# Kernel optimization log

Hardware: AMD Instinct MI355X
Metric: run time of the kernel (lower is better)

## Reference

```python
import jax, jax.numpy as jnp
import numpy as np
from jax.ops import segment_sum

N_NODES = 200000
N_EDGES = 3200000
N_GRAPHS = 400
IN_FEATS = 32
DIMS = [(32, 128), (128, 48), (48, 28), (28, 5)]  # (in, out) per SAGEConv layer


def setup_inputs() -> dict:
    key = jax.random.key(0)
    ks = jax.random.split(key, 4 + 3 * len(DIMS))
    inp = {
        'feat': jax.random.normal(ks[0], (N_NODES, IN_FEATS), dtype=jnp.float32),
        'src': jax.random.randint(ks[1], (N_EDGES,), 0, N_NODES),
        'dst': jax.random.randint(ks[2], (N_EDGES,), 0, N_NODES),
        'graph_ids': jnp.sort(jax.random.randint(ks[3], (N_NODES,), 0, N_GRAPHS)),
    }
    for i, (d_in, d_out) in enumerate(DIMS):
        s = 1.0 / np.sqrt(d_in)
        inp[f'W_self{i}'] = jax.random.uniform(ks[4 + 3 * i], (d_in, d_out), jnp.float32, -s, s)
        inp[f'W_neigh{i}'] = jax.random.uniform(ks[5 + 3 * i], (d_in, d_out), jnp.float32, -s, s)
        inp[f'b{i}'] = jax.random.uniform(ks[6 + 3 * i], (d_out,), jnp.float32, -s, s)
    return inp


def _sage_mean(h, src, dst, W_neigh, W_self, b):
    # mean-aggregate in-neighbor features, then project: fc_self(h) + fc_neigh(mean_u->v h_u) + b
    deg = segment_sum(jnp.ones((src.shape[0],), h.dtype), dst, num_segments=N_NODES)
    agg = segment_sum(h[src], dst, num_segments=N_NODES)  # [N, d_in] irregular gather+scatter
    agg = agg / jnp.maximum(deg, 1.0)[:, None]            # zero for isolated nodes (DGL semantics)
    return h @ W_self + agg @ W_neigh + b


def reference(feat, src, dst, graph_ids,
              W_self0, W_neigh0, b0, W_self1, W_neigh1, b1,
              W_self2, W_neigh2, b2, W_self3, W_neigh3, b3):
    h = jax.nn.relu(_sage_mean(feat, src, dst, W_neigh0, W_self0, b0))
    h = jax.nn.relu(_sage_mean(h, src, dst, W_neigh1, W_self1, b1))
    h = jax.nn.relu(_sage_mean(h, src, dst, W_neigh2, W_self2, b2))
    h = _sage_mean(h, src, dst, W_neigh3, W_self3, b3)
    # dgl.mean_nodes: per-graph mean readout
    cnt = segment_sum(jnp.ones((N_NODES,), h.dtype), graph_ids, num_segments=N_GRAPHS)
    tot = segment_sum(h, graph_ids, num_segments=N_GRAPHS)
    return tot / jnp.maximum(cnt, 1.0)[:, None]
```

## Files before the change

### kernel.cpp

```cpp
#include <hip/hip_runtime.h>

#define NN 200000
#define NE 3200000
#define NG 400
#define NB 196
#define BSHIFT 8
#define NBKT 782
#define EPB 12500
#define SRCMASK 0x3FFFF

__global__ void hist_bkt(const int* __restrict__ dst, int* __restrict__ bcnt) {
    __shared__ int h[NBKT];
    for (int i = threadIdx.x; i < NBKT; i += 256) h[i] = 0;
    __syncthreads();
    int stride = gridDim.x * blockDim.x;
    for (int e = blockIdx.x * blockDim.x + threadIdx.x; e < NE; e += stride)
        atomicAdd(&h[dst[e] >> BSHIFT], 1);
    __syncthreads();
    for (int i = threadIdx.x; i < NBKT; i += 256)
        if (h[i]) atomicAdd(&bcnt[i], h[i]);
}

__global__ void scan_bkt(const int* __restrict__ bcnt, int* __restrict__ bbase,
                         int* __restrict__ bcur) {
    __shared__ int sh[256];
    int t = threadIdx.x;
    int v[4]; int own = 0;
    #pragma unroll
    for (int i = 0; i < 4; ++i) {
        int idx = t * 4 + i;
        v[i] = (idx < NBKT) ? bcnt[idx] : 0;
        own += v[i];
    }
    sh[t] = own; __syncthreads();
    for (int off = 1; off < 256; off <<= 1) {
        int x = (t >= off) ? sh[t - off] : 0;
        __syncthreads();
        sh[t] += x;
        __syncthreads();
    }
    int excl = sh[t] - own;
    #pragma unroll
    for (int i = 0; i < 4; ++i) {
        int idx = t * 4 + i;
        if (idx < NBKT) { bbase[idx] = excl; bcur[idx] = excl; excl += v[i]; }
    }
}

__global__ void partition_pairs(const int* __restrict__ src, const int* __restrict__ dst,
                                int* __restrict__ bcur, unsigned int* __restrict__ pairs) {
    __shared__ int h[NBKT];
    __shared__ int base[NBKT];
    int e0 = blockIdx.x * EPB;
    int e1 = min(e0 + EPB, NE);
    for (int i = threadIdx.x; i < NBKT; i += 256) h[i] = 0;
    __syncthreads();
    for (int e = e0 + threadIdx.x; e < e1; e += 256)
        atomicAdd(&h[dst[e] >> BSHIFT], 1);
    __syncthreads();
    for (int i = threadIdx.x; i < NBKT; i += 256) {
        int c = h[i];
        base[i] = c ? atomicAdd(&bcur[i], c) : 0;
        h[i] = 0;
    }
    __syncthreads();
    for (int e = e0 + threadIdx.x; e < e1; e += 256) {
        int d = dst[e];
        int bk = d >> BSHIFT;
        int off = atomicAdd(&h[bk], 1);
        pairs[base[bk] + off] =
            ((unsigned int)(d & ((1 << BSHIFT) - 1)) << 18) | (unsigned int)src[e];
    }
}

__global__ void bucket_deg(const unsigned int* __restrict__ pairs,
                           const int* __restrict__ bbase, const int* __restrict__ bcur,
                           int* __restrict__ deg, float* __restrict__ inv) {
    __shared__ int h[1 << BSHIFT];
    int bk = blockIdx.x;
    h[threadIdx.x] = 0;
    __syncthreads();
    int p0 = bbase[bk], p1 = bcur[bk];
    for (int i = p0 + threadIdx.x; i < p1; i += 256)
        atomicAdd(&h[pairs[i] >> 18], 1);
    __syncthreads();
    int n = (bk << BSHIFT) + threadIdx.x;
    if (n < NN) {
        int d = h[threadIdx.x];
        deg[n] = d;
        inv[n] = 1.0f / fmaxf((float)d, 1.0f);
    }
}

__global__ void chunk_sums(const int* __restrict__ deg, int* __restrict__ bsum) {
    __shared__ int red[256];
    int b = blockIdx.x, t = threadIdx.x;
    int base = b * 1024 + t;
    int s = 0;
    #pragma unroll
    for (int i = 0; i < 4; ++i) { int idx = base + i * 256; if (idx < NN) s += deg[idx]; }
    red[t] = s; __syncthreads();
    for (int off = 128; off > 0; off >>= 1) {
        if (t < off) red[t] += red[t + off];
        __syncthreads();
    }
    if (t == 0) bsum[b] = red[0];
}

__global__ void scan_bsums(int* __restrict__ bsum, int* __restrict__ row_ptr) {
    __shared__ int sh[256];
    int t = threadIdx.x;
    int own = (t < NB) ? bsum[t] : 0;
    sh[t] = own; __syncthreads();
    for (int off = 1; off < 256; off <<= 1) {
        int v = (t >= off) ? sh[t - off] : 0;
        __syncthreads();
        sh[t] += v;
        __syncthreads();
    }
    if (t < NB) bsum[t] = sh[t] - own;
    if (t == 0) row_ptr[NN] = NE;
}

__global__ void scan_write(const int* __restrict__ deg, const int* __restrict__ bsum,
                           int* __restrict__ row_ptr) {
    __shared__ int sh[256];
    int b = blockIdx.x, t = threadIdx.x;
    int base = b * 1024 + t * 4;
    int v0 = (base     < NN) ? deg[base]     : 0;
    int v1 = (base + 1 < NN) ? deg[base + 1] : 0;
    int v2 = (base + 2 < NN) ? deg[base + 2] : 0;
    int v3 = (base + 3 < NN) ? deg[base + 3] : 0;
    int own = v0 + v1 + v2 + v3;
    sh[t] = own; __syncthreads();
    for (int off = 1; off < 256; off <<= 1) {
        int x = (t >= off) ? sh[t - off] : 0;
        __syncthreads();
        sh[t] += x;
        __syncthreads();
    }
    int excl = sh[t] - own + bsum[b];
    if (base     < NN) { row_ptr[base]     = excl; excl += v0; }
    if (base + 1 < NN) { row_ptr[base + 1] = excl; excl += v1; }
    if (base + 2 < NN) { row_ptr[base + 2] = excl; excl += v2; }
    if (base + 3 < NN) { row_ptr[base + 3] = excl; }
}

__global__ void bucket_scatter(const unsigned int* __restrict__ pairs,
                               const int* __restrict__ bbase, const int* __restrict__ bcur,
                               const int* __restrict__ row_ptr, int* __restrict__ csr_src) {
    __shared__ int cur[1 << BSHIFT];
    int bk = blockIdx.x;
    int n0 = bk << BSHIFT;
    int nend = min(n0 + (1 << BSHIFT), NN);
    if (threadIdx.x < nend - n0) cur[threadIdx.x] = row_ptr[n0 + threadIdx.x];
    __syncthreads();
    int p0 = bbase[bk], p1 = bcur[bk];
    for (int i = p0 + threadIdx.x; i < p1; i += 256) {
        unsigned int pr = pairs[i];
        int pos = atomicAdd(&cur[pr >> 18], 1);
        csr_src[pos] = (int)(pr & SRCMASK);
    }
}

template<int D, bool COMBINE, bool RELU>
__global__ void gather_lds_v4(const int* __restrict__ rp, const int* __restrict__ cs,
                              const float* __restrict__ xn, const float* __restrict__ hs,
                              const float* __restrict__ bias, const float* __restrict__ inv,
                              float* __restrict__ out) {
    constexpr int Q = D / 4;
    constexpr int NPB = 256 / Q;
    constexpr int CAP = 4096;
    __shared__ int shIdx[CAP];
    int n0 = blockIdx.x * NPB;
    if (n0 >= NN) return;
    int nEnd = min(n0 + NPB, NN);
    int e0 = rp[n0];
    int cnt = rp[nEnd] - e0;
    bool useLds = (cnt <= CAP);
    if (useLds)
        for (int i = threadIdx.x; i < cnt; i += 256) shIdx[i] = cs[e0 + i];
    __syncthreads();
    int t = threadIdx.x;
    int q = t % Q, l = t / Q;
    int n = n0 + l;
    if (l >= NPB || n >= NN) return;
    int s = rp[n] - e0, e = rp[n + 1] - e0;
    float4 acc = make_float4(0.f, 0.f, 0.f, 0.f);
    if (useLds) {
        int j = s;
        for (; j + 2 <= e; j += 2) {
            int s0 = shIdx[j], s1 = shIdx[j + 1];
            float4 a = *(const float4*)(xn + (size_t)s0 * D + q * 4);
            float4 b = *(const float4*)(xn + (size_t)s1 * D + q * 4);
            acc.x += a.x + b.x; acc.y += a.y + b.y;
            acc.z += a.z + b.z; acc.w += a.w + b.w;
        }
        if (j < e) {
            float4 a = *(const float4*)(xn + (size_t)shIdx[j] * D + q * 4);
            acc.x += a.x; acc.y += a.y; acc.z += a.z; acc.w += a.w;
        }
    } else {
        int j = s;
        for (; j + 2 <= e; j += 2) {
            int s0 = cs[e0 + j], s1 = cs[e0 + j + 1];
            float4 a = *(const float4*)(xn + (size_t)s0 * D + q * 4);
            float4 b = *(const float4*)(xn + (size_t)s1 * D + q * 4);
            acc.x += a.x + b.x; acc.y += a.y + b.y;
            acc.z += a.z + b.z; acc.w += a.w + b.w;
        }
        if (j < e) {
            float4 a = *(const float4*)(xn + (size_t)cs[e0 + j] * D + q * 4);
            acc.x += a.x; acc.y += a.y; acc.z += a.z; acc.w += a.w;
        }
    }
    size_t oidx = (size_t)n * D + q * 4;
    if (COMBINE) {
        float iv = inv[n];
        float4 h = *(const float4*)(hs + oidx);
        float4 bb = *(const float4*)(bias + q * 4);
        float4 r;
        r.x = h.x + iv * acc.x + bb.x;
        r.y = h.y + iv * acc.y + bb.y;
        r.z = h.z + iv * acc.z + bb.z;
        r.w = h.w + iv * acc.w + bb.w;
        if (RELU) {
            r.x = fmaxf(r.x, 0.f); r.y = fmaxf(r.y, 0.f);
            r.z = fmaxf(r.z, 0.f); r.w = fmaxf(r.w, 0.f);
        }
        *(float4*)(out + oidx) = r;
    } else {
        *(float4*)(out + oidx) = acc;
    }
}

__global__ void gather_lds_s5(const int* __restrict__ rp, const int* __restrict__ cs,
                              const float* __restrict__ xn, const float* __restrict__ hs,
                              const float* __restrict__ bias, const float* __restrict__ inv,
                              float* __restrict__ out) {
    constexpr int D = 5, Q = 5, NPB = 51, CAP = 4096;
    __shared__ int shIdx[CAP];
    int n0 = blockIdx.x * NPB;
    if (n0 >= NN) return;
    int nEnd = min(n0 + NPB, NN);
    int e0 = rp[n0];
    int cnt = rp[nEnd] - e0;
    bool useLds = (cnt <= CAP);
    if (useLds)
        for (int i = threadIdx.x; i < cnt; i += 256) shIdx[i] = cs[e0 + i];
    __syncthreads();
    int t = threadIdx.x;
    int q = t % Q, l = t / Q;
    int n = n0 + l;
    if (l >= NPB || n >= NN) return;
    int s = rp[n] - e0, e = rp[n + 1] - e0;
    float acc = 0.f;
    if (useLds) {
        int j = s;
        for (; j + 2 <= e; j += 2)
            acc += xn[(size_t)shIdx[j] * D + q] + xn[(size_t)shIdx[j + 1] * D + q];
        if (j < e) acc += xn[(size_t)shIdx[j] * D + q];
    } else {
        int j = s;
        for (; j + 2 <= e; j += 2)
            acc += xn[(size_t)cs[e0 + j] * D + q] + xn[(size_t)cs[e0 + j + 1] * D + q];
        if (j < e) acc += xn[(size_t)cs[e0 + j] * D + q];
    }
    size_t oidx = (size_t)n * D + q;
    out[oidx] = hs[oidx] + inv[n] * acc + bias[q];
}

template<int DIN, int DOUT, int NPER>
__global__ void proj_dual_lds(const float* __restrict__ h,
                              const float* __restrict__ Ws, const float* __restrict__ Wn,
                              float* __restrict__ hs, float* __restrict__ hn) {
    constexpr int Q = DOUT / 4;
    constexpr int GROUPS = 256 / Q;
    constexpr int NPB = GROUPS * NPER;
    __shared__ float4 shW[DIN * 2 * Q];
    const float4* Ws4 = (const float4*)Ws;
    const float4* Wn4 = (const float4*)Wn;
    for (int i = threadIdx.x; i < DIN * Q; i += 256) {
        int k = i / Q, q = i - k * Q;
        shW[k * 2 * Q + q]     = Ws4[i];
        shW[k * 2 * Q + Q + q] = Wn4[i];
    }
    __syncthreads();
    int t = threadIdx.x;
    int q = t % Q, g = t / Q;
    if (g >= GROUPS) return;
    int n0 = blockIdx.x * NPB + g * NPER;
    if (n0 >= NN) return;

    if (n0 + NPER <= NN) {
        float4 aS[NPER], aN[NPER];
        #pragma unroll
        for (int i = 0; i < NPER; ++i) {
            aS[i] = make_float4(0.f, 0.f, 0.f, 0.f);
            aN[i] = make_float4(0.f, 0.f, 0.f, 0.f);
        }
        const float* hp = h + (size_t)n0 * DIN;
        for (int kk = 0; kk < DIN; kk += 4) {
            float4 hv[NPER];
            #pragma unroll
            for (int i = 0; i < NPER; ++i)
                hv[i] = *(const float4*)(hp + (size_t)i * DIN + kk);
            #pragma unroll
            for (int dk = 0; dk < 4; ++dk) {
                float4 ws = shW[(kk + dk) * 2 * Q + q];
                float4 wn = shW[(kk + dk) * 2 * Q + Q + q];
                #pragma unroll
                for (int i = 0; i < NPER; ++i) {
                    float v = ((const float*)&hv[i])[dk];
                    aS[i].x = fmaf(v, ws.x, aS[i].x); aS[i].y = fmaf(v, ws.y, aS[i].y);
                    aS[i].z = fmaf(v, ws.z, aS[i].z); aS[i].w = fmaf(v, ws.w, aS[i].w);
                    aN[i].x = fmaf(v, wn.x, aN[i].x); aN[i].y = fmaf(v, wn.y, aN[i].y);
                    aN[i].z = fmaf(v, wn.z, aN[i].z); aN[i].w = fmaf(v, wn.w, aN[i].w);
                }
            }
        }
        #pragma unroll
        for (int i = 0; i < NPER; ++i) {
            *(float4*)(hs + (size_t)(n0 + i) * DOUT + q * 4) = aS[i];
            *(float4*)(hn + (size_t)(n0 + i) * DOUT + q * 4) = aN[i];
        }
    } else {
        for (int i = 0; i < NPER; ++i) {
            int n = n0 + i;
            if (n >= NN) break;
            float4 aS = make_float4(0.f, 0.f, 0.f, 0.f);
            float4 aN = make_float4(0.f, 0.f, 0.f, 0.f);
            const float* hp = h + (size_t)n * DIN;
            for (int kk = 0; kk < DIN; kk += 4) {
                float4 hv = *(const float4*)(hp + kk);
                #pragma unroll
                for (int dk = 0; dk < 4; ++dk) {
                    float4 ws = shW[(kk + dk) * 2 * Q + q];
                    float4 wn = shW[(kk + dk) * 2 * Q + Q + q];
                    float v = ((const float*)&hv)[dk];
                    aS.x = fmaf(v, ws.x, aS.x); aS.y = fmaf(v, ws.y, aS.y);
                    aS.z = fmaf(v, ws.z, aS.z); aS.w = fmaf(v, ws.w, aS.w);
                    aN.x = fmaf(v, wn.x, aN.x); aN.y = fmaf(v, wn.y, aN.y);
                    aN.z = fmaf(v, wn.z, aN.z); aN.w = fmaf(v, wn.w, aN.w);
                }
            }
            *(float4*)(hs + (size_t)n * DOUT + q * 4) = aS;
            *(float4*)(hn + (size_t)n * DOUT + q * 4) = aN;
        }
    }
}

template<int DIN, int DOUT>
__global__ void proj_dual_s(const float* __restrict__ h,
                            const float* __restrict__ Ws, const float* __restrict__ Wn,
                            float* __restrict__ hs, float* __restrict__ hn) {
    const int total = NN * DOUT;
    int tid = blockIdx.x * blockDim.x + threadIdx.x;
    if (tid >= total) return;
    int n = tid / DOUT, j = tid - n * DOUT;
    const float* r = h + (size_t)n * DIN;
    float aS = 0.f, aN = 0.f;
    #pragma unroll 4
    for (int k = 0; k < DIN; ++k) {
        float v = r[k];
        aS = fmaf(v, Ws[k * DOUT + j], aS);
        aN = fmaf(v, Wn[k * DOUT + j], aN);
    }
    hs[tid] = aS;
    hn[tid] = aN;
}

__global__ void layer0_lds(const float* __restrict__ feat, const float* __restrict__ agg,
                           const float* __restrict__ Ws, const float* __restrict__ Wn,
                           const float* __restrict__ bias, const float* __restrict__ inv,
                           float* __restrict__ out) {
    constexpr int DIN = 32, DOUT = 128, Q = 32, NPER = 4;
    constexpr int NPB = 8 * NPER;
    __shared__ float4 shW[DIN * 2 * Q];
    const float4* Ws4 = (const float4*)Ws;
    const float4* Wn4 = (const float4*)Wn;
    for (int i = threadIdx.x; i < DIN * Q; i += 256) {
        int k = i / Q, q = i - k * Q;
        shW[k * 2 * Q + q]     = Ws4[i];
        shW[k * 2 * Q + Q + q] = Wn4[i];
    }
    __syncthreads();
    int t = threadIdx.x;
    int q = t & 31, g = t >> 5;
    int n0 = blockIdx.x * NPB + g * NPER;
    if (n0 >= NN) return;
    float4 bb = *(const float4*)(bias + q * 4);

    if (n0 + NPER <= NN) {
        float4 aS[NPER], aN[NPER];
        #pragma unroll
        for (int i = 0; i < NPER; ++i) {
            aS[i] = make_float4(0.f, 0.f, 0.f, 0.f);
            aN[i] = make_float4(0.f, 0.f, 0.f, 0.f);
        }
        const float* fp = feat + (size_t)n0 * DIN;
        const float* ap = agg + (size_t)n0 * DIN;
        for (int kk = 0; kk < DIN; kk += 4) {
            float4 fv[NPER], av[NPER];
            #pragma unroll
            for (int i = 0; i < NPER; ++i) {
                fv[i] = *(const float4*)(fp + (size_t)i * DIN + kk);
                av[i] = *(const float4*)(ap + (size_t)i * DIN + kk);
            }
            #pragma unroll
            for (int dk = 0; dk < 4; ++dk) {
                float4 ws = shW[(kk + dk) * 2 * Q + q];
                float4 wn = shW[(kk + dk) * 2 * Q + Q + q];
                #pragma unroll
                for (int i = 0; i < NPER; ++i) {
                    float f = ((const float*)&fv[i])[dk];
                    float a = ((const float*)&av[i])[dk];
                    aS[i].x = fmaf(f, ws.x, aS[i].x); aS[i].y = fmaf(f, ws.y, aS[i].y);
                    aS[i].z = fmaf(f, ws.z, aS[i].z); aS[i].w = fmaf(f, ws.w, aS[i].w);
                    aN[i].x = fmaf(a, wn.x, aN[i].x); aN[i].y = fmaf(a, wn.y, aN[i].y);
                    aN[i].z = fmaf(a, wn.z, aN[i].z); aN[i].w = fmaf(a, wn.w, aN[i].w);
                }
            }
        }
        #pragma unroll
        for (int i = 0; i < NPER; ++i) {
            float iv = inv[n0 + i];
            float4 r;
            r.x = fmaxf(aS[i].x + iv * aN[i].x + bb.x, 0.f);
            r.y = fmaxf(aS[i].y + iv * aN[i].y + bb.y, 0.f);
            r.z = fmaxf(aS[i].z + iv * aN[i].z + bb.z, 0.f);
            r.w = fmaxf(aS[i].w + iv * aN[i].w + bb.w, 0.f);
            *(float4*)(out + (size_t)(n0 + i) * DOUT + q * 4) = r;
        }
    } else {
        for (int i = 0; i < NPER; ++i) {
            int n = n0 + i;
            if (n >= NN) break;
            float4 aS = make_float4(0.f, 0.f, 0.f, 0.f);
            float4 aN = make_float4(0.f, 0.f, 0.f, 0.f);
            for (int kk = 0; kk < DIN; kk += 4) {
                float4 fv = *(const float4*)(feat + (size_t)n * DIN + kk);
                float4 av = *(const float4*)(agg + (size_t)n * DIN + kk);
                #pragma unroll
                for (int dk = 0; dk < 4; ++dk) {
                    float4 ws = shW[(kk + dk) * 2 * Q + q];
                    float4 wn = shW[(kk + dk) * 2 * Q + Q + q];
                    float f = ((const float*)&fv)[dk];
                    float a = ((const float*)&av)[dk];
                    aS.x = fmaf(f, ws.x, aS.x); aS.y = fmaf(f, ws.y, aS.y);
                    aS.z = fmaf(f, ws.z, aS.z); aS.w = fmaf(f, ws.w, aS.w);
                    aN.x = fmaf(a, wn.x, aN.x); aN.y = fmaf(a, wn.y, aN.y);
                    aN.z = fmaf(a, wn.z, aN.z); aN.w = fmaf(a, wn.w, aN.w);
                }
            }
            float iv = inv[n];
            float4 r;
            r.x = fmaxf(aS.x + iv * aN.x + bb.x, 0.f);
            r.y = fmaxf(aS.y + iv * aN.y + bb.y, 0.f);
            r.z = fmaxf(aS.z + iv * aN.z + bb.z, 0.f);
            r.w = fmaxf(aS.w + iv * aN.w + bb.w, 0.f);
            *(float4*)(out + (size_t)n * DOUT + q * 4) = r;
        }
    }
}

__global__ void readout_graph(const float* __restrict__ h, const int* __restrict__ gid,
                              float* __restrict__ out) {
    const int g = blockIdx.x;
    const int t = threadIdx.x;
    int lo = 0, hi = NN;
    while (lo < hi) { int mid = (lo + hi) >> 1; if (gid[mid] < g) lo = mid + 1; else hi = mid; }
    const int start = lo;
    hi = NN;
    while (lo < hi) { int mid = (lo + hi) >> 1; if (gid[mid] <= g) lo = mid + 1; else hi = mid; }
    const int end = lo;

    float acc[5] = {0.f, 0.f, 0.f, 0.f, 0.f};
    for (int n = start + t; n < end; n += blockDim.x) {
        const float* row = h + (size_t)n * 5;
        #pragma unroll
        for (int j = 0; j < 5; ++j) acc[j] += row[j];
    }
    __shared__ float sh[5][256];
    #pragma unroll
    for (int j = 0; j < 5; ++j) sh[j][t] = acc[j];
    __syncthreads();
    for (int off = 128; off > 0; off >>= 1) {
        if (t < off) {
            #pragma unroll
            for (int j = 0; j < 5; ++j) sh[j][t] += sh[j][t + off];
        }
        __syncthreads();
    }
    if (t < 5) {
        float cnt = (float)(end - start);
        out[g * 5 + t] = sh[t][0] / fmaxf(cnt, 1.f);
    }
}

extern "C" void kernel_launch(void* const* d_in, const int* in_sizes, int n_in,
                              void* d_out, int out_size, void* d_ws, size_t ws_size,
                              hipStream_t stream) {
    const float* feat = (const float*)d_in[0];
    const int*   src  = (const int*)d_in[1];
    const int*   dst  = (const int*)d_in[2];
    const int*   gid  = (const int*)d_in[3];
    const float* Ws0 = (const float*)d_in[4],  *Wn0 = (const float*)d_in[5],  *b0 = (const float*)d_in[6];
    const float* Ws1 = (const float*)d_in[7],  *Wn1 = (const float*)d_in[8],  *b1 = (const float*)d_in[9];
    const float* Ws2 = (const float*)d_in[10], *Wn2 = (const float*)d_in[11], *b2 = (const float*)d_in[12];
    const float* Ws3 = (const float*)d_in[13], *Wn3 = (const float*)d_in[14], *b3 = (const float*)d_in[15];
    float* out = (float*)d_out;

    float* ws   = (float*)d_ws;
    float* inv  = ws;
    float* bufA = inv  + NN;
    float* bufB = bufA + (size_t)NN * 128;
    float* bufC = bufB + (size_t)NN * 48;
    int*   deg     = (int*)(bufC + (size_t)NN * 48);
    int*   row_ptr = deg + NN;
    int*   bsum    = row_ptr + NN + 1;
    int*   bcnt    = bsum + 256;
    int*   bbase   = bcnt + NBKT;
    int*   bcur    = bbase + NBKT;
    int*   csr_src = bcur + NBKT;
    unsigned int* pairs = (unsigned int*)bufB;

    const dim3 blk(256);

    hipMemsetAsync(bcnt, 0, NBKT * sizeof(int), stream);
    hist_bkt<<<512, blk, 0, stream>>>(dst, bcnt);
    scan_bkt<<<1, blk, 0, stream>>>(bcnt, bbase, bcur);
    partition_pairs<<<(NE + EPB - 1) / EPB, blk, 0, stream>>>(src, dst, bcur, pairs);
    bucket_deg<<<NBKT, blk, 0, stream>>>(pairs, bbase, bcur, deg, inv);
    chunk_sums<<<NB, blk, 0, stream>>>(deg, bsum);
    scan_bsums<<<1, blk, 0, stream>>>(bsum, row_ptr);
    scan_write<<<NB, blk, 0, stream>>>(deg, bsum, row_ptr);
    bucket_scatter<<<NBKT, blk, 0, stream>>>(pairs, bbase, bcur, row_ptr, csr_src);

    gather_lds_v4<32, false, false><<<(NN + 31) / 32, blk, 0, stream>>>(
        row_ptr, csr_src, feat, nullptr, nullptr, nullptr, bufB);
    layer0_lds<<<(NN + 31) / 32, blk, 0, stream>>>(feat, bufB, Ws0, Wn0, b0, inv, bufA);

    proj_dual_lds<128, 48, 4><<<(NN + 83) / 84, blk, 0, stream>>>(bufA, Ws1, Wn1, bufB, bufC);
    gather_lds_v4<48, true, true><<<(NN + 20) / 21, blk, 0, stream>>>(
        row_ptr, csr_src, bufC, bufB, b1, inv, bufA);

    proj_dual_lds<48, 28, 4><<<(NN + 143) / 144, blk, 0, stream>>>(bufA, Ws2, Wn2, bufB, bufC);
    gather_lds_v4<28, true, true><<<(NN + 35) / 36, blk, 0, stream>>>(
        row_ptr, csr_src, bufC, bufB, b2, inv, bufA);

    proj_dual_s<28, 5><<<(NN * 5 + 255) / 256, blk, 0, stream>>>(bufA, Ws3, Wn3, bufB, bufC);
    gather_lds_s5<<<(NN + 50) / 51, blk, 0, stream>>>(row_ptr, csr_src, bufC, bufB, b3, inv, bufA);

    readout_graph<<<NG, blk, 0, stream>>>(bufA, gid, out);
}
```

Before: 769.9 us.

## Store neighbor-gather features in fp16 to halve irregular gather traffic

The per-edge neighbor feature gathers now read fp16 rows instead of fp32 and still accumulate in fp32. Layer 0 gets an extra conversion kernel that turns the input features into fp16. The projection kernels write the neighbor projection directly as fp16. The 28-wide layer is padded to a 32-wide stride so each row loads as aligned 8-half vectors, and the downstream kernels read that stride. This targets the memory bandwidth of the random row gathers over 3.2M edges, at the cost of fp16 rounding error in the aggregated features and one extra pass over the input features.

```diff
diff --git a/kernel.cpp b/kernel.cpp
--- a/kernel.cpp
+++ b/kernel.cpp
@@ -8,6 +8,8 @@
 #define NBKT 782
 #define EPB 12500
 #define SRCMASK 0x3FFFF
+
+typedef _Float16 half_t;
 
 __global__ void hist_bkt(const int* __restrict__ dst, int* __restrict__ bcnt) {
     __shared__ int h[NBKT];
@@ -163,12 +165,22 @@
     }
 }
 
-template<int D, bool COMBINE, bool RELU>
-__global__ void gather_lds_v4(const int* __restrict__ rp, const int* __restrict__ cs,
-                              const float* __restrict__ xn, const float* __restrict__ hs,
-                              const float* __restrict__ bias, const float* __restrict__ inv,
-                              float* __restrict__ out) {
-    constexpr int Q = D / 4;
+__global__ void f32_to_h8(const float* __restrict__ in, half_t* __restrict__ out, int total8) {
+    int tid = blockIdx.x * blockDim.x + threadIdx.x;
+    if (tid >= total8) return;
+    const float4 a = ((const float4*)in)[tid * 2];
+    const float4 b = ((const float4*)in)[tid * 2 + 1];
+    union { uint4 u; half_t h[8]; } r;
+    r.h[0] = (half_t)a.x; r.h[1] = (half_t)a.y; r.h[2] = (half_t)a.z; r.h[3] = (half_t)a.w;
+    r.h[4] = (half_t)b.x; r.h[5] = (half_t)b.y; r.h[6] = (half_t)b.z; r.h[7] = (half_t)b.w;
+    ((uint4*)out)[tid] = r.u;
+}
+
+template<int DH, int Q, int MODE>
+__global__ void gather_h(const int* __restrict__ rp, const int* __restrict__ cs,
+                         const half_t* __restrict__ xn, const float* __restrict__ hs,
+                         const float* __restrict__ bias, const float* __restrict__ inv,
+                         float* __restrict__ out) {
     constexpr int NPB = 256 / Q;
     constexpr int CAP = 4096;
     __shared__ int shIdx[CAP];
@@ -186,51 +198,63 @@
     int n = n0 + l;
     if (l >= NPB || n >= NN) return;
     int s = rp[n] - e0, e = rp[n + 1] - e0;
-    float4 acc = make_float4(0.f, 0.f, 0.f, 0.f);
+    float acc[8] = {0.f, 0.f, 0.f, 0.f, 0.f, 0.f, 0.f, 0.f};
+    union H8 { uint4 u; half_t h[8]; };
     if (useLds) {
         int j = s;
         for (; j + 2 <= e; j += 2) {
-            int s0 = shIdx[j], s1 = shIdx[j + 1];
-            float4 a = *(const float4*)(xn + (size_t)s0 * D + q * 4);
-            float4 b = *(const float4*)(xn + (size_t)s1 * D + q * 4);
-            acc.x += a.x + b.x; acc.y += a.y + b.y;
-            acc.z += a.z + b.z; acc.w += a.w + b.w;
+            H8 a, b;
+            a.u = *(const uint4*)(xn + (size_t)shIdx[j]     * DH + q * 8);
+            b.u = *(const uint4*)(xn + (size_t)shIdx[j + 1] * DH + q * 8);
+            #pragma unroll
+            for (int k = 0; k < 8; ++k) acc[k] += (float)a.h[k] + (float)b.h[k];
         }
         if (j < e) {
-            float4 a = *(const float4*)(xn + (size_t)shIdx[j] * D + q * 4);
-            acc.x += a.x; acc.y += a.y; acc.z += a.z; acc.w += a.w;
+            H8 a; a.u = *(const uint4*)(xn + (size_t)shIdx[j] * DH + q * 8);
+            #pragma unroll
+            for (int k = 0; k < 8; ++k) acc[k] += (float)a.h[k];
         }
     } else {
         int j = s;
         for (; j + 2 <= e; j += 2) {
-            int s0 = cs[e0 + j], s1 = cs[e0 + j + 1];
-            float4 a = *(const float4*)(xn + (size_t)s0 * D + q * 4);
-            float4 b = *(const float4*)(xn + (size_t)s1 * D + q * 4);
-            acc.x += a.x + b.x; acc.y += a.y + b.y;
-            acc.z += a.z + b.z; acc.w += a.w + b.w;
+            H8 a, b;
+            a.u = *(const uint4*)(xn + (size_t)cs[e0 + j]     * DH + q * 8);
+            b.u = *(const uint4*)(xn + (size_t)cs[e0 + j + 1] * DH + q * 8);
+            #pragma unroll
+            for (int k = 0; k < 8; ++k) acc[k] += (float)a.h[k] + (float)b.h[k];
         }
         if (j < e) {
-            float4 a = *(const float4*)(xn + (size_t)cs[e0 + j] * D + q * 4);
-            acc.x += a.x; acc.y += a.y; acc.z += a.z; acc.w += a.w;
-        }
-    }
-    size_t oidx = (size_t)n * D + q * 4;
-    if (COMBINE) {
+            H8 a; a.u = *(const uint4*)(xn + (size_t)cs[e0 + j] * DH + q * 8);
+            #pragma unroll
+            for (int k = 0; k < 8; ++k) acc[k] += (float)a.h[k];
+        }
+    }
+    size_t base = (size_t)n * DH + q * 8;
+    if (MODE == 0) {
+        float4 r0 = make_float4(acc[0], acc[1], acc[2], acc[3]);
+        float4 r1 = make_float4(acc[4], acc[5], acc[6], acc[7]);
+        *(float4*)(out + base)     = r0;
+        *(float4*)(out + base + 4) = r1;
+    } else {
         float iv = inv[n];
-        float4 h = *(const float4*)(hs + oidx);
-        float4 bb = *(const float4*)(bias + q * 4);
-        float4 r;
-        r.x = h.x + iv * acc.x + bb.x;
-        r.y = h.y + iv * acc.y + bb.y;
-        r.z = h.z + iv * acc.z + bb.z;
-        r.w = h.w + iv * acc.w + bb.w;
-        if (RELU) {
-            r.x = fmaxf(r.x, 0.f); r.y = fmaxf(r.y, 0.f);
-            r.z = fmaxf(r.z, 0.f); r.w = fmaxf(r.w, 0.f);
-        }
-        *(float4*)(out + oidx) = r;
-    } else {
-        *(float4*)(out + oidx) = acc;
+        float4 h0 = *(const float4*)(hs + base);
+        float4 b0 = *(const float4*)(bias + q * 8);
+        float4 r0;
+        r0.x = fmaxf(h0.x + iv * acc[0] + b0.x, 0.f);
+        r0.y = fmaxf(h0.y + iv * acc[1] + b0.y, 0.f);
+        r0.z = fmaxf(h0.z + iv * acc[2] + b0.z, 0.f);
+        r0.w = fmaxf(h0.w + iv * acc[3] + b0.w, 0.f);
+        *(float4*)(out + base) = r0;
+        if (MODE == 1 || q < Q - 1) {
+            float4 h1 = *(const float4*)(hs + base + 4);
+            float4 b1 = *(const float4*)(bias + q * 8 + 4);
+            float4 r1;
+            r1.x = fmaxf(h1.x + iv * acc[4] + b1.x, 0.f);
+            r1.y = fmaxf(h1.y + iv * acc[5] + b1.y, 0.f);
+            r1.z = fmaxf(h1.z + iv * acc[6] + b1.z, 0.f);
+            r1.w = fmaxf(h1.w + iv * acc[7] + b1.w, 0.f);
+            *(float4*)(out + base + 4) = r1;
+        }
     }
 }
 
@@ -270,10 +294,10 @@
     out[oidx] = hs[oidx] + inv[n] * acc + bias[q];
 }
 
-template<int DIN, int DOUT, int NPER>
-__global__ void proj_dual_lds(const float* __restrict__ h,
-                              const float* __restrict__ Ws, const float* __restrict__ Wn,
-                              float* __restrict__ hs, float* __restrict__ hn) {
+template<int DIN, int DINS, int DOUT, int DOUTS, int NPER>
+__global__ void proj_dual_lds_h(const float* __restrict__ h,
+                                const float* __restrict__ Ws, const float* __restrict__ Wn,
+                                float* __restrict__ hs, half_t* __restrict__ hn) {
     constexpr int Q = DOUT / 4;
     constexpr int GROUPS = 256 / Q;
     constexpr int NPB = GROUPS * NPER;
@@ -291,6 +315,19 @@
     if (g >= GROUPS) return;
     int n0 = blockIdx.x * NPB + g * NPER;
     if (n0 >= NN) return;
+    union H4 { unsigned long long u; half_t hh[4]; };
+
+    auto emit = [&](int n, const float4& aS, const float4& aN) {
+        *(float4*)(hs + (size_t)n * DOUTS + q * 4) = aS;
+        H4 r;
+        r.hh[0] = (half_t)aN.x; r.hh[1] = (half_t)aN.y;
+        r.hh[2] = (half_t)aN.z; r.hh[3] = (half_t)aN.w;
+        *(unsigned long long*)(hn + (size_t)n * DOUTS + q * 4) = r.u;
+        if (DOUTS > DOUT && q == Q - 1) {
+            H4 z; z.u = 0ull;
+            *(unsigned long long*)(hn + (size_t)n * DOUTS + DOUT) = z.u;
+        }
+    };
 
     if (n0 + NPER <= NN) {
         float4 aS[NPER], aN[NPER];
@@ -299,12 +336,12 @@
             aS[i] = make_float4(0.f, 0.f, 0.f, 0.f);
             aN[i] = make_float4(0.f, 0.f, 0.f, 0.f);
         }
-        const float* hp = h + (size_t)n0 * DIN;
+        const float* hp = h + (size_t)n0 * DINS;
         for (int kk = 0; kk < DIN; kk += 4) {
             float4 hv[NPER];
             #pragma unroll
             for (int i = 0; i < NPER; ++i)
-                hv[i] = *(const float4*)(hp + (size_t)i * DIN + kk);
+                hv[i] = *(const float4*)(hp + (size_t)i * DINS + kk);
             #pragma unroll
             for (int dk = 0; dk < 4; ++dk) {
                 float4 ws = shW[(kk + dk) * 2 * Q + q];
@@ -320,17 +357,14 @@
             }
         }
         #pragma unroll
-        for (int i = 0; i < NPER; ++i) {
-            *(float4*)(hs + (size_t)(n0 + i) * DOUT + q * 4) = aS[i];
-            *(float4*)(hn + (size_t)(n0 + i) * DOUT + q * 4) = aN[i];
-        }
+        for (int i = 0; i < NPER; ++i) emit(n0 + i, aS[i], aN[i]);
     } else {
         for (int i = 0; i < NPER; ++i) {
             int n = n0 + i;
             if (n >= NN) break;
             float4 aS = make_float4(0.f, 0.f, 0.f, 0.f);
             float4 aN = make_float4(0.f, 0.f, 0.f, 0.f);
-            const float* hp = h + (size_t)n * DIN;
+            const float* hp = h + (size_t)n * DINS;
             for (int kk = 0; kk < DIN; kk += 4) {
                 float4 hv = *(const float4*)(hp + kk);
                 #pragma unroll
@@ -344,13 +378,12 @@
                     aN.z = fmaf(v, wn.z, aN.z); aN.w = fmaf(v, wn.w, aN.w);
                 }
             }
-            *(float4*)(hs + (size_t)n * DOUT + q * 4) = aS;
-            *(float4*)(hn + (size_t)n * DOUT + q * 4) = aN;
-        }
-    }
-}
-
-template<int DIN, int DOUT>
+            emit(n, aS, aN);
+        }
+    }
+}
+
+template<int DINS, int DIN, int DOUT>
 __global__ void proj_dual_s(const float* __restrict__ h,
                             const float* __restrict__ Ws, const float* __restrict__ Wn,
                             float* __restrict__ hs, float* __restrict__ hn) {
@@ -358,7 +391,7 @@
     int tid = blockIdx.x * blockDim.x + threadIdx.x;
     if (tid >= total) return;
     int n = tid / DOUT, j = tid - n * DOUT;
-    const float* r = h + (size_t)n * DIN;
+    const float* r = h + (size_t)n * DINS;
     float aS = 0.f, aN = 0.f;
     #pragma unroll 4
     for (int k = 0; k < DIN; ++k) {
@@ -524,6 +557,8 @@
     int*   bcur    = bbase + NBKT;
     int*   csr_src = bcur + NBKT;
     unsigned int* pairs = (unsigned int*)bufB;
+    half_t* hbuf  = (half_t*)bufC;
+    float*  hn5   = bufC;
 
     const dim3 blk(256);
 
@@ -537,20 +572,23 @@
     scan_write<<<NB, blk, 0, stream>>>(deg, bsum, row_ptr);
     bucket_scatter<<<NBKT, blk, 0, stream>>>(pairs, bbase, bcur, row_ptr, csr_src);
 
-    gather_lds_v4<32, false, false><<<(NN + 31) / 32, blk, 0, stream>>>(
-        row_ptr, csr_src, feat, nullptr, nullptr, nullptr, bufB);
+    f32_to_h8<<<(NN * 4 + 255) / 256, blk, 0, stream>>>(feat, hbuf, NN * 4);
+    gather_h<32, 4, 0><<<(NN + 63) / 64, blk, 0, stream>>>(
+        row_ptr, csr_src, hbuf, nullptr, nullptr, nullptr, bufB);
     layer0_lds<<<(NN + 31) / 32, blk, 0, stream>>>(feat, bufB, Ws0, Wn0, b0, inv, bufA);
 
-    proj_dual_lds<128, 48, 4><<<(NN + 83) / 84, blk, 0, stream>>>(bufA, Ws1, Wn1, bufB, bufC);
-    gather_lds_v4<48, true, true><<<(NN + 20) / 21, blk, 0, stream>>>(
-        row_ptr, csr_src, bufC, bufB, b1, inv, bufA);
-
-    proj_dual_lds<48, 28, 4><<<(NN + 143) / 144, blk, 0, stream>>>(bufA, Ws2, Wn2, bufB, bufC);
-    gather_lds_v4<28, true, true><<<(NN + 35) / 36, blk, 0, stream>>>(
-        row_ptr, csr_src, bufC, bufB, b2, inv, bufA);
-
-    proj_dual_s<28, 5><<<(NN * 5 + 255) / 256, blk, 0, stream>>>(bufA, Ws3, Wn3, bufB, bufC);
-    gather_lds_s5<<<(NN + 50) / 51, blk, 0, stream>>>(row_ptr, csr_src, bufC, bufB, b3, inv, bufA);
+    proj_dual_lds_h<128, 128, 48, 48, 4><<<(NN + 83) / 84, blk, 0, stream>>>(
+        bufA, Ws1, Wn1, bufB, hbuf);
+    gather_h<48, 6, 1><<<(NN + 41) / 42, blk, 0, stream>>>(
+        row_ptr, csr_src, hbuf, bufB, b1, inv, bufA);
+
+    proj_dual_lds_h<48, 48, 28, 32, 4><<<(NN + 143) / 144, blk, 0, stream>>>(
+        bufA, Ws2, Wn2, bufB, hbuf);
+    gather_h<32, 4, 2><<<(NN + 63) / 64, blk, 0, stream>>>(
+        row_ptr, csr_src, hbuf, bufB, b2, inv, bufA);
+
+    proj_dual_s<32, 28, 5><<<(NN * 5 + 255) / 256, blk, 0, stream>>>(bufA, Ws3, Wn3, bufB, hn5);
+    gather_lds_s5<<<(NN + 50) / 51, blk, 0, stream>>>(row_ptr, csr_src, hn5, bufB, b3, inv, bufA);
 
     readout_graph<<<NG, blk, 0, stream>>>(bufA, gid, out);
 }
```

Result: faster. 685.8 us (-10.9%).
